# Performance work log

Measured on AMD Instinct MI355X. Metric: run time of the kernel, lower is better.

## Reference

```python
import jax, jax.numpy as jnp
import numpy as np

# config constants
B, S, H = 4, 2048, 1024
E = 8                 # n_routed_experts
M = 512               # moe_intermediate_size
K = 2                 # num_experts_per_tok
N_SHARED = 2
SM = M * N_SHARED     # shared expert intermediate
G = 64                # gene_size
GE_TEMP = 1.0
ALPHA = 0.001         # aux_loss_alpha
SEQ_AUX = True
NORM_TOPK = True
COS_TEMP = 0.78
CONS_ALPHA = 0.01
LEAKY_SLOPE = 0.01
EPS_COS = 1e-8


def setup_inputs() -> dict:
    key = jax.random.key(0)
    ks = jax.random.split(key, 12)
    sh = 1.0 / np.sqrt(H)
    sm = 1.0 / np.sqrt(M)
    ssm = 1.0 / np.sqrt(SM)
    sg = 1.0 / np.sqrt(G)
    return {
        "hidden_states": jax.random.normal(ks[0], (B, S, H), jnp.float32),
        "g": jax.random.normal(ks[1], (B, G), jnp.float32),
        "wt": jax.random.uniform(ks[2], (E, H), jnp.float32, -sh, sh),   # gate weight_token
        "wg": jax.random.uniform(ks[3], (E, G), jnp.float32, -sg, sg),   # gate weight_gene
        "w_gate": jax.random.uniform(ks[4], (E, H, M), jnp.float32, -sh, sh),
        "w_up": jax.random.uniform(ks[5], (E, H, M), jnp.float32, -sh, sh),
        "w_down": jax.random.uniform(ks[6], (E, M, H), jnp.float32, -sm, sm),
        "sw_gate": jax.random.uniform(ks[7], (H, SM), jnp.float32, -sh, sh),
        "sw_up": jax.random.uniform(ks[8], (H, SM), jnp.float32, -sh, sh),
        "sw_down": jax.random.uniform(ks[9], (SM, H), jnp.float32, -ssm, ssm),
    }


def _leaky(x):
    return jnp.where(x >= 0, x, LEAKY_SLOPE * x)


def _moe_forward(hidden_states, g, wt, wg, w_gate, w_up, w_down, sw_gate, sw_up, sw_down):
    b, s, h = hidden_states.shape
    x = hidden_states.reshape(-1, h)                    # [T, H], T = b*s
    T = x.shape[0]

    # ---- gate ----
    logits_h = x @ wt.T                                 # [T, E]
    logits_g = g @ wg.T                                 # [b, E]
    logits_g = jnp.repeat(logits_g, s, axis=0)          # [T, E]
    logits = (logits_h + logits_g / GE_TEMP) / (1.0 + 1.0 / GE_TEMP)
    scores = jax.nn.softmax(logits, axis=-1)            # [T, E]
    topk_w, topk_idx = jax.lax.top_k(scores, K)         # [T, K]
    if K > 1 and NORM_TOPK:
        topk_w = topk_w / (topk_w.sum(-1, keepdims=True) + 1e-20)

    # aux loss (seq_aux=True)
    onehot = jax.nn.one_hot(topk_idx.reshape(b, s * K), E, dtype=jnp.float32)  # [b, s*K, E]
    ce = onehot.sum(1) / (s * K / E)                    # [b, E]
    aux_loss = (ce * scores.reshape(b, s, E).mean(1)).sum(1).mean() * ALPHA

    # ---- routed experts: dense stacked compute, then gather ----
    gp = _leaky(jnp.einsum('th,ehm->etm', x, w_gate))   # [E, T, M]
    up = jnp.einsum('th,ehm->etm', x, w_up)
    y_all = jnp.einsum('etm,emh->eth', gp * up, w_down) # [E, T, H]
    y_sel = y_all[topk_idx, jnp.arange(T)[:, None], :]  # [T, K, H]
    y = (y_sel * topk_w[..., None]).sum(1).reshape(b, s, h)

    # ---- shared expert ----
    p = (_leaky(hidden_states @ sw_gate) * (hidden_states @ sw_up)) @ sw_down
    y = y + p

    # consistency cosine loss
    num = jnp.sum(y * p, -1)
    den = jnp.maximum(jnp.linalg.norm(y, axis=-1), EPS_COS) * jnp.maximum(jnp.linalg.norm(p, axis=-1), EPS_COS)
    closs = CONS_ALPHA * jnp.mean((num / den) / (1.0 + COS_TEMP))
    return y, aux_loss + closs


def reference(hidden_states, g, wt, wg, w_gate, w_up, w_down, sw_gate, sw_up, sw_down):
    y, _ = _moe_forward(hidden_states, g, wt, wg, w_gate, w_up, w_down, sw_gate, sw_up, sw_down)
    return y
```

## Files before the change

kernel.cpp:

```cpp
#include <hip/hip_runtime.h>
#include <stdint.h>

#define T_TOK 8192
#define H_DIM 1024
#define M_DIM 512
#define SM_DIM 1024
#define E_NUM 8
#define S_SEQ 2048
#define G_DIM 64
#define NASSIGN 16384
#define NSLOT (NASSIGN + E_NUM * 128)
#define MAX_TILES (NASSIGN / 128 + E_NUM)
#define NBLK_PLACE (NASSIGN / 256)

typedef float f32x4 __attribute__((ext_vector_type(4)));
typedef short bf16x8 __attribute__((ext_vector_type(8)));

struct TileDesc { int base; int expert; int nrows; };

#define WAITCNT_VM4 asm volatile("s_waitcnt vmcnt(4)" ::: "memory")
#define WAITCNT_VM0 asm volatile("s_waitcnt vmcnt(0)" ::: "memory")
#define WAITCNT_LGKM0 asm volatile("s_waitcnt lgkmcnt(0)" ::: "memory")

static __device__ __forceinline__ ushort f2b(float f) {
  union { float f; uint32_t u; } a; a.f = f;
  uint32_t r = a.u + 0x7fffu + ((a.u >> 16) & 1u);
  return (ushort)(r >> 16);
}
static __device__ __forceinline__ float b2f(ushort u) {
  union { uint32_t u; float f; } a; a.u = ((uint32_t)u) << 16;
  return a.f;
}
static __device__ __forceinline__ int imin(int a, int b) { return a < b ? a : b; }

static __device__ __forceinline__ void gll16(const void* g, void* l) {
  __builtin_amdgcn_global_load_lds(
      (const __attribute__((address_space(1))) void*)g,
      (__attribute__((address_space(3))) void*)l, 16, 0, 0);
}
static __device__ __forceinline__ int swz(int row) { return (row >> 1) & 3; }
static __device__ __forceinline__ int xcd_remap(int wg, int nwg) {
  return (wg & 7) * (nwg >> 3) + (wg >> 3);
}

__global__ void cvt_x_kernel(const float* __restrict__ x, ushort* __restrict__ xb) {
  int i = blockIdx.x * 256 + threadIdx.x;
  const float4 v = ((const float4*)x)[i];
  ushort4 o;
  o.x = f2b(v.x); o.y = f2b(v.y); o.z = f2b(v.z); o.w = f2b(v.w);
  ((ushort4*)xb)[i] = o;
}

__global__ void tcvt_kernel(const float* __restrict__ src, ushort* __restrict__ dst, int R, int C) {
  __shared__ float tile[32][33];
  size_t bo = (size_t)blockIdx.z * R * C;
  src += bo; dst += bo;
  int c0 = blockIdx.x * 32, r0 = blockIdx.y * 32;
#pragma unroll
  for (int i = 0; i < 4; ++i)
    tile[threadIdx.y + i * 8][threadIdx.x] =
        src[(size_t)(r0 + threadIdx.y + i * 8) * C + c0 + threadIdx.x];
  __syncthreads();
#pragma unroll
  for (int i = 0; i < 4; ++i)
    dst[(size_t)(c0 + threadIdx.y + i * 8) * R + r0 + threadIdx.x] =
        f2b(tile[threadIdx.x][threadIdx.y + i * 8]);
}

__global__ void lg_kernel(const float* __restrict__ g, const float* __restrict__ wg,
                          float* __restrict__ lg) {
  int tid = threadIdx.x;
  if (tid < 4 * E_NUM) {
    int b = tid >> 3, e = tid & 7;
    float s = 0.f;
    for (int i = 0; i < G_DIM; ++i) s += g[b * G_DIM + i] * wg[e * G_DIM + i];
    lg[tid] = s;
  }
}

__global__ __launch_bounds__(64) void router_kernel(
    const float* __restrict__ x, const float* __restrict__ wt, const float* __restrict__ lg,
    int* __restrict__ tidx, float* __restrict__ tw) {
  int t = blockIdx.x;
  int lane = threadIdx.x;
  const float* xr = x + (size_t)t * H_DIM;
  float a[E_NUM];
#pragma unroll
  for (int e = 0; e < E_NUM; ++e) a[e] = 0.f;
  for (int i = lane; i < H_DIM; i += 64) {
    float xv = xr[i];
#pragma unroll
    for (int e = 0; e < E_NUM; ++e) a[e] += xv * wt[e * H_DIM + i];
  }
#pragma unroll
  for (int e = 0; e < E_NUM; ++e)
    for (int off = 32; off; off >>= 1) a[e] += __shfl_xor(a[e], off, 64);
  if (lane == 0) {
    int b = t / S_SEQ;
    float l[E_NUM];
#pragma unroll
    for (int e = 0; e < E_NUM; ++e) l[e] = 0.5f * (a[e] + lg[b * E_NUM + e]);
    int i1 = 0; float b1 = l[0];
#pragma unroll
    for (int e = 1; e < E_NUM; ++e) if (l[e] > b1) { b1 = l[e]; i1 = e; }
    int i2 = -1; float b2 = -1e30f;
#pragma unroll
    for (int e = 0; e < E_NUM; ++e) if (e != i1 && l[e] > b2) { b2 = l[e]; i2 = e; }
    float e2 = expf(b2 - b1);
    float inv = 1.f / (1.f + e2);
    tidx[t * 2] = i1; tidx[t * 2 + 1] = i2;
    tw[t * 2] = inv;  tw[t * 2 + 1] = e2 * inv;
  }
}

__global__ __launch_bounds__(256) void hist_kernel(const int* __restrict__ tidx,
                                                   int* __restrict__ bcount) {
  __shared__ int h[E_NUM];
  int tid = threadIdx.x;
  if (tid < E_NUM) h[tid] = 0;
  __syncthreads();
  atomicAdd(&h[tidx[blockIdx.x * 256 + tid]], 1);
  __syncthreads();
  if (tid < E_NUM) bcount[blockIdx.x * E_NUM + tid] = h[tid];
}

__global__ __launch_bounds__(64) void scan2_kernel(
    const int* __restrict__ bcount, int* __restrict__ boffs, int* __restrict__ offs,
    TileDesc* __restrict__ desc, int* __restrict__ ndesc) {
  __shared__ int cnt[E_NUM];
  __shared__ int off_s[E_NUM];
  int lane = threadIdx.x;
  if (lane < E_NUM) {
    int s = 0;
    for (int b = 0; b < NBLK_PLACE; ++b) s += bcount[b * E_NUM + lane];
    cnt[lane] = s;
  }
  __syncthreads();
  if (lane == 0) {
    int o = 0, nd = 0;
    for (int e = 0; e < E_NUM; ++e) {
      off_s[e] = o;
      offs[e] = o;
      int n = cnt[e];
      for (int tb = 0; tb < n; tb += 128) {
        desc[nd].base = o + tb; desc[nd].expert = e;
        desc[nd].nrows = imin(n - tb, 128);
        ++nd;
      }
      o += n;
    }
    offs[E_NUM] = o;
    *ndesc = nd;
  }
  __syncthreads();
  if (lane < E_NUM) {
    int run = off_s[lane];
    for (int b = 0; b < NBLK_PLACE; ++b) {
      boffs[b * E_NUM + lane] = run;
      run += bcount[b * E_NUM + lane];
    }
  }
}

__global__ __launch_bounds__(256) void place2_kernel(
    const int* __restrict__ tidx, const int* __restrict__ boffs,
    int* __restrict__ perm, int* __restrict__ slot_of) {
  __shared__ int wcnt[4][E_NUM];
  int tid = threadIdx.x, wv = tid >> 6, lane = tid & 63;
  int i = blockIdx.x * 256 + tid;
  int e = tidx[i];
  unsigned long long lower = (lane == 63) ? 0x7fffffffffffffffull : ((1ull << lane) - 1ull);
  int rank = 0;
#pragma unroll
  for (int ee = 0; ee < E_NUM; ++ee) {
    unsigned long long m = __ballot(e == ee);
    if (e == ee) rank = __popcll(m & lower);
    if (lane == 0) wcnt[wv][ee] = __popcll(m);
  }
  __syncthreads();
  int off = boffs[blockIdx.x * E_NUM + e];
  for (int w = 0; w < wv; ++w) off += wcnt[w][e];
  int pos = off + rank;
  perm[pos] = i >> 1;
  slot_of[i] = pos;
}

__global__ __launch_bounds__(256) void gemm_dual_kernel(
    const ushort* __restrict__ A, const ushort* __restrict__ B0t, const ushort* __restrict__ B1t,
    ushort* __restrict__ Hout, int Kd, int Nd, int ncols,
    const int* __restrict__ perm, const TileDesc* __restrict__ desc, const int* __restrict__ ndesc) {
  __shared__ ushort As[2][128 * 32];
  __shared__ ushort B0s[2][64 * 32];
  __shared__ ushort B1s[2][64 * 32];

  int id = xcd_remap(blockIdx.x, gridDim.x);
  int mt = id / ncols, n0 = (id % ncols) * 64;

  int rowbase, nrows;
  const ushort *b0g, *b1g;
  if (desc) {
    if (mt >= *ndesc) return;
    TileDesc d = desc[mt];
    rowbase = d.base; nrows = d.nrows;
    size_t wo = (size_t)d.expert * Nd * Kd;
    b0g = B0t + wo; b1g = B1t + wo;
  } else {
    rowbase = mt * 128; nrows = 128; b0g = B0t; b1g = B1t;
  }
  int tid = threadIdx.x;
  int wv = tid >> 6, lane = tid & 63;

  int l4 = lane >> 2, c = lane & 3;
  int a0 = wv * 16 + l4, a1 = a0 + 64;
  int ga0 = desc ? perm[rowbase + imin(a0, nrows - 1)] : (rowbase + a0);
  int ga1 = desc ? perm[rowbase + imin(a1, nrows - 1)] : (rowbase + a1);
  const ushort* ap0 = A + (size_t)ga0 * Kd + ((c ^ swz(a0)) << 3);
  const ushort* ap1 = A + (size_t)ga1 * Kd + ((c ^ swz(a1)) << 3);
  int br = wv * 16 + l4;
  const ushort* bp0 = b0g + (size_t)(n0 + br) * Kd + ((c ^ swz(br)) << 3);
  const ushort* bp1 = b1g + (size_t)(n0 + br) * Kd + ((c ^ swz(br)) << 3);

  int wr = wv >> 1, wc = wv & 1;
  int lr = lane & 15, cg = lane >> 4;

  f32x4 acc0[4][2], acc1[4][2];
#pragma unroll
  for (int m = 0; m < 4; ++m)
#pragma unroll
    for (int n = 0; n < 2; ++n) { acc0[m][n] = (f32x4){0.f,0.f,0.f,0.f}; acc1[m][n] = (f32x4){0.f,0.f,0.f,0.f}; }

  int nk = Kd >> 5;
  gll16(ap0, &As[0][wv * 512]); gll16(ap1, &As[0][(wv + 4) * 512]);
  gll16(bp0, &B0s[0][wv * 512]); gll16(bp1, &B1s[0][wv * 512]);
  ap0 += 32; ap1 += 32; bp0 += 32; bp1 += 32;

  for (int kt = 0; kt < nk; ++kt) {
    int cur = kt & 1, nxt = cur ^ 1;
    if (kt + 1 < nk) {
      gll16(ap0, &As[nxt][wv * 512]); gll16(ap1, &As[nxt][(wv + 4) * 512]);
      gll16(bp0, &B0s[nxt][wv * 512]); gll16(bp1, &B1s[nxt][wv * 512]);
      ap0 += 32; ap1 += 32; bp0 += 32; bp1 += 32;
      WAITCNT_VM4;
    } else {
      WAITCNT_VM0;
    }
    __builtin_amdgcn_s_barrier();
    bf16x8 af[4], bq0[2], bq1[2];
#pragma unroll
    for (int m = 0; m < 4; ++m) {
      int row = wr * 64 + m * 16 + lr;
      af[m] = *(const bf16x8*)&As[cur][row * 32 + ((cg ^ swz(row)) << 3)];
    }
#pragma unroll
    for (int n = 0; n < 2; ++n) {
      int row = wc * 32 + n * 16 + lr;
      bq0[n] = *(const bf16x8*)&B0s[cur][row * 32 + ((cg ^ swz(row)) << 3)];
      bq1[n] = *(const bf16x8*)&B1s[cur][row * 32 + ((cg ^ swz(row)) << 3)];
    }
    WAITCNT_LGKM0;
    __builtin_amdgcn_s_barrier();
#pragma unroll
    for (int m = 0; m < 4; ++m)
#pragma unroll
      for (int n = 0; n < 2; ++n) {
        acc0[m][n] = __builtin_amdgcn_mfma_f32_16x16x32_bf16(af[m], bq0[n], acc0[m][n], 0, 0, 0);
        acc1[m][n] = __builtin_amdgcn_mfma_f32_16x16x32_bf16(af[m], bq1[n], acc1[m][n], 0, 0, 0);
      }
  }
  int rq = cg * 4, cq = lr;
#pragma unroll
  for (int m = 0; m < 4; ++m)
#pragma unroll
    for (int n = 0; n < 2; ++n)
#pragma unroll
      for (int r = 0; r < 4; ++r) {
        int row = wr * 64 + m * 16 + rq + r;
        if (row < nrows) {
          float gv = acc0[m][n][r], uv = acc1[m][n][r];
          float hv = (gv >= 0.f ? gv : 0.01f * gv) * uv;
          int col = n0 + wc * 32 + n * 16 + cq;
          Hout[(size_t)(rowbase + row) * Nd + col] = f2b(hv);
        }
      }
}

template <int BF16OUT>
__global__ __launch_bounds__(256) void gemm_single_kernel(
    const ushort* __restrict__ A, const ushort* __restrict__ Bt, void* __restrict__ Out,
    int Kd, int Nd, int ncols, const TileDesc* __restrict__ desc, const int* __restrict__ ndesc) {
  __shared__ ushort As[2][128 * 32];
  __shared__ ushort Bs[2][128 * 32];

  int id = xcd_remap(blockIdx.x, gridDim.x);
  int mt = id / ncols, n0 = (id % ncols) * 128;

  int rowbase, nrows;
  const ushort* bg;
  if (desc) {
    if (mt >= *ndesc) return;
    TileDesc d = desc[mt];
    rowbase = d.base; nrows = d.nrows;
    bg = Bt + (size_t)d.expert * Nd * Kd;
  } else {
    rowbase = mt * 128; nrows = 128; bg = Bt;
  }
  int tid = threadIdx.x;
  int wv = tid >> 6, lane = tid & 63;

  int l4 = lane >> 2, c = lane & 3;
  int a0 = wv * 16 + l4, a1 = a0 + 64;
  const ushort* ap0 = A + (size_t)(rowbase + a0) * Kd + ((c ^ swz(a0)) << 3);
  const ushort* ap1 = A + (size_t)(rowbase + a1) * Kd + ((c ^ swz(a1)) << 3);
  const ushort* bp0 = bg + (size_t)(n0 + a0) * Kd + ((c ^ swz(a0)) << 3);
  const ushort* bp1 = bg + (size_t)(n0 + a1) * Kd + ((c ^ swz(a1)) << 3);

  int wr = wv >> 1, wc = wv & 1;
  int lr = lane & 15, cg = lane >> 4;

  f32x4 acc[4][4];
#pragma unroll
  for (int m = 0; m < 4; ++m)
#pragma unroll
    for (int n = 0; n < 4; ++n) acc[m][n] = (f32x4){0.f,0.f,0.f,0.f};

  int nk = Kd >> 5;
  gll16(ap0, &As[0][wv * 512]); gll16(ap1, &As[0][(wv + 4) * 512]);
  gll16(bp0, &Bs[0][wv * 512]); gll16(bp1, &Bs[0][(wv + 4) * 512]);
  ap0 += 32; ap1 += 32; bp0 += 32; bp1 += 32;

  for (int kt = 0; kt < nk; ++kt) {
    int cur = kt & 1, nxt = cur ^ 1;
    if (kt + 1 < nk) {
      gll16(ap0, &As[nxt][wv * 512]); gll16(ap1, &As[nxt][(wv + 4) * 512]);
      gll16(bp0, &Bs[nxt][wv * 512]); gll16(bp1, &Bs[nxt][(wv + 4) * 512]);
      ap0 += 32; ap1 += 32; bp0 += 32; bp1 += 32;
      WAITCNT_VM4;
    } else {
      WAITCNT_VM0;
    }
    __builtin_amdgcn_s_barrier();
    bf16x8 af[4], bfr[4];
#pragma unroll
    for (int m = 0; m < 4; ++m) {
      int row = wr * 64 + m * 16 + lr;
      af[m] = *(const bf16x8*)&As[cur][row * 32 + ((cg ^ swz(row)) << 3)];
    }
#pragma unroll
    for (int n = 0; n < 4; ++n) {
      int row = wc * 64 + n * 16 + lr;
      bfr[n] = *(const bf16x8*)&Bs[cur][row * 32 + ((cg ^ swz(row)) << 3)];
    }
    WAITCNT_LGKM0;
    __builtin_amdgcn_s_barrier();
#pragma unroll
    for (int m = 0; m < 4; ++m)
#pragma unroll
      for (int n = 0; n < 4; ++n)
        acc[m][n] = __builtin_amdgcn_mfma_f32_16x16x32_bf16(af[m], bfr[n], acc[m][n], 0, 0, 0);
  }
  int rq = cg * 4, cq = lr;
#pragma unroll
  for (int m = 0; m < 4; ++m)
#pragma unroll
    for (int n = 0; n < 4; ++n)
#pragma unroll
      for (int r = 0; r < 4; ++r) {
        int row = wr * 64 + m * 16 + rq + r;
        if (row < nrows) {
          int col = n0 + wc * 64 + n * 16 + cq;
          size_t o = (size_t)(rowbase + row) * Nd + col;
          if (BF16OUT) ((ushort*)Out)[o] = f2b(acc[m][n][r]);
          else ((float*)Out)[o] = acc[m][n][r];
        }
      }
}

__global__ void final_kernel(float* __restrict__ y, const ushort* __restrict__ ye,
                             const int* __restrict__ slot_of, const float* __restrict__ tw) {
  int i = blockIdx.x * 256 + threadIdx.x;
  int t = i >> 8;
  int c4 = (i & 255) * 4;
  int s0 = slot_of[t * 2], s1 = slot_of[t * 2 + 1];
  float w0 = tw[t * 2], w1 = tw[t * 2 + 1];
  float4 v = ((float4*)y)[i];
  ushort4 a = *(const ushort4*)(ye + (size_t)s0 * H_DIM + c4);
  ushort4 b = *(const ushort4*)(ye + (size_t)s1 * H_DIM + c4);
  v.x += w0 * b2f(a.x) + w1 * b2f(b.x);
  v.y += w0 * b2f(a.y) + w1 * b2f(b.y);
  v.z += w0 * b2f(a.z) + w1 * b2f(b.z);
  v.w += w0 * b2f(a.w) + w1 * b2f(b.w);
  ((float4*)y)[i] = v;
}

extern "C" void kernel_launch(void* const* d_in, const int* in_sizes, int n_in,
                              void* d_out, int out_size, void* d_ws, size_t ws_size,
                              hipStream_t stream) {
  const float* x       = (const float*)d_in[0];
  const float* g       = (const float*)d_in[1];
  const float* wt      = (const float*)d_in[2];
  const float* wg      = (const float*)d_in[3];
  const float* w_gate  = (const float*)d_in[4];
  const float* w_up    = (const float*)d_in[5];
  const float* w_down  = (const float*)d_in[6];
  const float* sw_gate = (const float*)d_in[7];
  const float* sw_up   = (const float*)d_in[8];
  const float* sw_down = (const float*)d_in[9];
  float* y = (float*)d_out;

  char* p = (char*)d_ws;
  auto alloc = [&](size_t bytes) -> char* {
    char* r = p;
    p += (bytes + 255) & ~(size_t)255;
    return r;
  };
  ushort* xb    = (ushort*)alloc((size_t)T_TOK * H_DIM * 2);
  ushort* wg_t  = (ushort*)alloc((size_t)E_NUM * M_DIM * H_DIM * 2);
  ushort* wu_t  = (ushort*)alloc((size_t)E_NUM * M_DIM * H_DIM * 2);
  ushort* wd_t  = (ushort*)alloc((size_t)E_NUM * H_DIM * M_DIM * 2);
  ushort* swg_t = (ushort*)alloc((size_t)SM_DIM * H_DIM * 2);
  ushort* swu_t = (ushort*)alloc((size_t)SM_DIM * H_DIM * 2);
  ushort* swd_t = (ushort*)alloc((size_t)H_DIM * SM_DIM * 2);
  float* lg     = (float*)alloc(4 * E_NUM * 4);
  int* tidx     = (int*)alloc(NASSIGN * 4);
  float* tw     = (float*)alloc(NASSIGN * 4);
  int* bcount   = (int*)alloc(NBLK_PLACE * E_NUM * 4);
  int* boffs    = (int*)alloc(NBLK_PLACE * E_NUM * 4);
  int* offs     = (int*)alloc((E_NUM + 1) * 4);
  int* ndesc    = (int*)alloc(4);
  int* perm     = (int*)alloc(NASSIGN * 4);
  int* slot_of  = (int*)alloc(NASSIGN * 4);
  TileDesc* desc = (TileDesc*)alloc(MAX_TILES * sizeof(TileDesc));
  ushort* h_e   = (ushort*)alloc((size_t)NSLOT * M_DIM * 2);
  ushort* hsh   = (ushort*)alloc((size_t)T_TOK * SM_DIM * 2);
  ushort* ye    = (ushort*)alloc((size_t)NSLOT * H_DIM * 2);
  (void)ws_size; (void)in_sizes; (void)n_in; (void)out_size;

  cvt_x_kernel<<<T_TOK * H_DIM / 4 / 256, 256, 0, stream>>>(x, xb);
  dim3 tb(32, 8);
  tcvt_kernel<<<dim3(M_DIM / 32, H_DIM / 32, E_NUM), tb, 0, stream>>>(w_gate, wg_t, H_DIM, M_DIM);
  tcvt_kernel<<<dim3(M_DIM / 32, H_DIM / 32, E_NUM), tb, 0, stream>>>(w_up, wu_t, H_DIM, M_DIM);
  tcvt_kernel<<<dim3(H_DIM / 32, M_DIM / 32, E_NUM), tb, 0, stream>>>(w_down, wd_t, M_DIM, H_DIM);
  tcvt_kernel<<<dim3(SM_DIM / 32, H_DIM / 32, 1), tb, 0, stream>>>(sw_gate, swg_t, H_DIM, SM_DIM);
  tcvt_kernel<<<dim3(SM_DIM / 32, H_DIM / 32, 1), tb, 0, stream>>>(sw_up, swu_t, H_DIM, SM_DIM);
  tcvt_kernel<<<dim3(H_DIM / 32, SM_DIM / 32, 1), tb, 0, stream>>>(sw_down, swd_t, SM_DIM, H_DIM);

  lg_kernel<<<1, 32, 0, stream>>>(g, wg, lg);
  router_kernel<<<T_TOK, 64, 0, stream>>>(x, wt, lg, tidx, tw);
  hist_kernel<<<NBLK_PLACE, 256, 0, stream>>>(tidx, bcount);
  scan2_kernel<<<1, 64, 0, stream>>>(bcount, boffs, offs, desc, ndesc);
  place2_kernel<<<NBLK_PLACE, 256, 0, stream>>>(tidx, boffs, perm, slot_of);

  gemm_dual_kernel<<<(T_TOK / 128) * (SM_DIM / 64), 256, 0, stream>>>(
      xb, swg_t, swu_t, hsh, H_DIM, SM_DIM, SM_DIM / 64, nullptr, nullptr, nullptr);
  gemm_single_kernel<0><<<(T_TOK / 128) * (H_DIM / 128), 256, 0, stream>>>(
      hsh, swd_t, (void*)y, SM_DIM, H_DIM, H_DIM / 128, nullptr, nullptr);

  gemm_dual_kernel<<<MAX_TILES * (M_DIM / 64), 256, 0, stream>>>(
      xb, wg_t, wu_t, h_e, H_DIM, M_DIM, M_DIM / 64, perm, desc, ndesc);
  gemm_single_kernel<1><<<MAX_TILES * (H_DIM / 128), 256, 0, stream>>>(
      h_e, wd_t, (void*)ye, M_DIM, H_DIM, H_DIM / 128, desc, ndesc);

  final_kernel<<<T_TOK * H_DIM / 4 / 256, 256, 0, stream>>>(y, ye, slot_of, tw);
}
```

Before: 241.5 us.

## Merge shared and routed GEMMs into combined launches with 256-row tiles and triple buffering

```diff
diff --git a/kernel.cpp b/kernel.cpp
--- a/kernel.cpp
+++ b/kernel.cpp
@@ -9,8 +9,8 @@
 #define S_SEQ 2048
 #define G_DIM 64
 #define NASSIGN 16384
-#define NSLOT (NASSIGN + E_NUM * 128)
-#define MAX_TILES (NASSIGN / 128 + E_NUM)
+#define NSLOT (NASSIGN + E_NUM * 256)
+#define MAX_TILES (NASSIGN / 256 + E_NUM)
 #define NBLK_PLACE (NASSIGN / 256)
 
 typedef float f32x4 __attribute__((ext_vector_type(4)));
@@ -19,6 +19,7 @@
 struct TileDesc { int base; int expert; int nrows; };
 
 #define WAITCNT_VM4 asm volatile("s_waitcnt vmcnt(4)" ::: "memory")
+#define WAITCNT_VM3 asm volatile("s_waitcnt vmcnt(3)" ::: "memory")
 #define WAITCNT_VM0 asm volatile("s_waitcnt vmcnt(0)" ::: "memory")
 #define WAITCNT_LGKM0 asm volatile("s_waitcnt lgkmcnt(0)" ::: "memory")
 
@@ -142,9 +143,9 @@
       off_s[e] = o;
       offs[e] = o;
       int n = cnt[e];
-      for (int tb = 0; tb < n; tb += 128) {
+      for (int tb = 0; tb < n; tb += 256) {
         desc[nd].base = o + tb; desc[nd].expert = e;
-        desc[nd].nrows = imin(n - tb, 128);
+        desc[nd].nrows = imin(n - tb, 256);
         ++nd;
       }
       o += n;
@@ -185,194 +186,218 @@
   slot_of[i] = pos;
 }
 
-__global__ __launch_bounds__(256) void gemm_dual_kernel(
-    const ushort* __restrict__ A, const ushort* __restrict__ B0t, const ushort* __restrict__ B1t,
-    ushort* __restrict__ Hout, int Kd, int Nd, int ncols,
-    const int* __restrict__ perm, const TileDesc* __restrict__ desc, const int* __restrict__ ndesc) {
-  __shared__ ushort As[2][128 * 32];
-  __shared__ ushort B0s[2][64 * 32];
-  __shared__ ushort B1s[2][64 * 32];
-
+template <int DUAL>
+static __device__ __forceinline__ void gemm_core(
+    const ushort* __restrict__ A, const ushort* __restrict__ B0,
+    const ushort* __restrict__ B1, void* __restrict__ Out, int outf32,
+    int Kd, int NdOut, int rowbase, int nrows, int n0,
+    const int* __restrict__ perm, ushort* Asb, ushort* Bsb) {
+  constexpr int BN = DUAL ? 256 : 128;
+  constexpr int BSTRIDE = BN * 32;
+  int tid = threadIdx.x, wv = tid >> 6, lane = tid & 63;
+  int sr = tid >> 2, sc = tid & 3;
+  int r1 = sr + 128;
+
+  int ga0 = perm ? perm[rowbase + imin(sr, nrows - 1)] : (rowbase + sr);
+  int ga1 = perm ? perm[rowbase + imin(r1, nrows - 1)] : (rowbase + r1);
+  const ushort* ap0 = A + (size_t)ga0 * Kd + ((sc ^ swz(sr)) << 3);
+  const ushort* ap1 = A + (size_t)ga1 * Kd + ((sc ^ swz(r1)) << 3);
+  const ushort* bp0;
+  const ushort* bp1 = nullptr;
+  if (DUAL) {
+    int rb0 = n0 + sr, rb1 = n0 + r1;
+    const ushort* s0 = ((rb0 >> 4) & 1) ? B1 : B0;
+    const ushort* s1 = ((rb1 >> 4) & 1) ? B1 : B0;
+    bp0 = s0 + (size_t)(((rb0 >> 5) << 4) + (rb0 & 15)) * Kd + ((sc ^ swz(sr)) << 3);
+    bp1 = s1 + (size_t)(((rb1 >> 5) << 4) + (rb1 & 15)) * Kd + ((sc ^ swz(r1)) << 3);
+  } else {
+    bp0 = B0 + (size_t)(n0 + sr) * Kd + ((sc ^ swz(sr)) << 3);
+  }
+
+  auto stageA = [&](int b) {
+    ushort* ad = Asb + b * 8192 + wv * 512;
+    gll16(ap0, ad); gll16(ap1, ad + 4096);
+    ap0 += 32; ap1 += 32;
+  };
+  auto stageB = [&](int b) {
+    ushort* bd = Bsb + b * BSTRIDE + wv * 512;
+    gll16(bp0, bd); bp0 += 32;
+    if (DUAL) { gll16(bp1, bd + 4096); bp1 += 32; }
+  };
+
+  int wr = wv >> 2, wc = wv & 3;
+  int lr = lane & 15, cg = lane >> 4;
+
+  constexpr int NF = DUAL ? 4 : 2;
+  f32x4 acc[8][NF];
+#pragma unroll
+  for (int m = 0; m < 8; ++m)
+#pragma unroll
+    for (int n = 0; n < NF; ++n) acc[m][n] = (f32x4){0.f, 0.f, 0.f, 0.f};
+
+  int nk = Kd >> 5;
+  stageA(0); stageB(0);
+  stageA(1); stageB(1);
+  if (DUAL) WAITCNT_VM4; else WAITCNT_VM3;
+  __builtin_amdgcn_s_barrier();
+
+  for (int kt = 0; kt < nk; ++kt) {
+    int b = kt % 3;
+    const ushort* abuf = Asb + b * 8192;
+    const ushort* bbuf = Bsb + b * BSTRIDE;
+    bool pf = (kt + 2 < nk);
+    int b2 = (kt + 2) % 3;
+
+    if (DUAL) {
+      bf16x8 af[8];
+#pragma unroll
+      for (int m = 0; m < 8; ++m) {
+        int row = wr * 128 + m * 16 + lr;
+        af[m] = *(const bf16x8*)(abuf + row * 32 + ((cg ^ swz(row)) << 3));
+      }
+      bf16x8 bq[2];
+#pragma unroll
+      for (int n = 0; n < 2; ++n) {
+        int row = wc * 64 + n * 16 + lr;
+        bq[n] = *(const bf16x8*)(bbuf + row * 32 + ((cg ^ swz(row)) << 3));
+      }
+      if (pf) stageA(b2);
+      __builtin_amdgcn_s_setprio(1);
+#pragma unroll
+      for (int m = 0; m < 8; ++m) {
+        acc[m][0] = __builtin_amdgcn_mfma_f32_16x16x32_bf16(af[m], bq[0], acc[m][0], 0, 0, 0);
+        acc[m][1] = __builtin_amdgcn_mfma_f32_16x16x32_bf16(af[m], bq[1], acc[m][1], 0, 0, 0);
+      }
+      __builtin_amdgcn_s_setprio(0);
+      bf16x8 bq2[2];
+#pragma unroll
+      for (int n = 0; n < 2; ++n) {
+        int row = wc * 64 + (n + 2) * 16 + lr;
+        bq2[n] = *(const bf16x8*)(bbuf + row * 32 + ((cg ^ swz(row)) << 3));
+      }
+      if (pf) stageB(b2);
+      __builtin_amdgcn_s_setprio(1);
+#pragma unroll
+      for (int m = 0; m < 8; ++m) {
+        acc[m][2] = __builtin_amdgcn_mfma_f32_16x16x32_bf16(af[m], bq2[0], acc[m][2], 0, 0, 0);
+        acc[m][3] = __builtin_amdgcn_mfma_f32_16x16x32_bf16(af[m], bq2[1], acc[m][3], 0, 0, 0);
+      }
+      __builtin_amdgcn_s_setprio(0);
+    } else {
+      bf16x8 bq[2];
+#pragma unroll
+      for (int n = 0; n < 2; ++n) {
+        int row = wc * 32 + n * 16 + lr;
+        bq[n] = *(const bf16x8*)(bbuf + row * 32 + ((cg ^ swz(row)) << 3));
+      }
+      bf16x8 af[4];
+#pragma unroll
+      for (int m = 0; m < 4; ++m) {
+        int row = wr * 128 + m * 16 + lr;
+        af[m] = *(const bf16x8*)(abuf + row * 32 + ((cg ^ swz(row)) << 3));
+      }
+      if (pf) { stageA(b2); stageB(b2); }
+      __builtin_amdgcn_s_setprio(1);
+#pragma unroll
+      for (int m = 0; m < 4; ++m) {
+        acc[m][0] = __builtin_amdgcn_mfma_f32_16x16x32_bf16(af[m], bq[0], acc[m][0], 0, 0, 0);
+        acc[m][1] = __builtin_amdgcn_mfma_f32_16x16x32_bf16(af[m], bq[1], acc[m][1], 0, 0, 0);
+      }
+      __builtin_amdgcn_s_setprio(0);
+      bf16x8 af2[4];
+#pragma unroll
+      for (int m = 0; m < 4; ++m) {
+        int row = wr * 128 + (m + 4) * 16 + lr;
+        af2[m] = *(const bf16x8*)(abuf + row * 32 + ((cg ^ swz(row)) << 3));
+      }
+      __builtin_amdgcn_s_setprio(1);
+#pragma unroll
+      for (int m = 0; m < 4; ++m) {
+        acc[m + 4][0] = __builtin_amdgcn_mfma_f32_16x16x32_bf16(af2[m], bq[0], acc[m + 4][0], 0, 0, 0);
+        acc[m + 4][1] = __builtin_amdgcn_mfma_f32_16x16x32_bf16(af2[m], bq[1], acc[m + 4][1], 0, 0, 0);
+      }
+      __builtin_amdgcn_s_setprio(0);
+    }
+    WAITCNT_LGKM0;
+    if (pf) { if (DUAL) WAITCNT_VM4; else WAITCNT_VM3; }
+    else WAITCNT_VM0;
+    __builtin_amdgcn_s_barrier();
+  }
+
+  int rq = cg * 4, cq = lr;
+  if (DUAL) {
+#pragma unroll
+    for (int m = 0; m < 8; ++m)
+#pragma unroll
+      for (int p = 0; p < 2; ++p)
+#pragma unroll
+        for (int r = 0; r < 4; ++r) {
+          int row = wr * 128 + m * 16 + rq + r;
+          if (row < nrows) {
+            float gv = acc[m][2 * p][r], uv = acc[m][2 * p + 1][r];
+            float hv = (gv >= 0.f ? gv : 0.01f * gv) * uv;
+            int col = (n0 >> 1) + wc * 32 + p * 16 + cq;
+            ((ushort*)Out)[(size_t)(rowbase + row) * NdOut + col] = f2b(hv);
+          }
+        }
+  } else {
+#pragma unroll
+    for (int m = 0; m < 8; ++m)
+#pragma unroll
+      for (int n = 0; n < 2; ++n)
+#pragma unroll
+        for (int r = 0; r < 4; ++r) {
+          int row = wr * 128 + m * 16 + rq + r;
+          if (row < nrows) {
+            int col = n0 + wc * 32 + n * 16 + cq;
+            size_t o = (size_t)(rowbase + row) * NdOut + col;
+            if (outf32) ((float*)Out)[o] = acc[m][n][r];
+            else ((ushort*)Out)[o] = f2b(acc[m][n][r]);
+          }
+        }
+  }
+}
+
+__global__ __launch_bounds__(512) void gemm_dual_all(
+    const ushort* __restrict__ xb, const ushort* __restrict__ swg,
+    const ushort* __restrict__ swu, ushort* __restrict__ hsh,
+    const ushort* __restrict__ wg, const ushort* __restrict__ wu,
+    ushort* __restrict__ h_e, const int* __restrict__ perm,
+    const TileDesc* __restrict__ desc, const int* __restrict__ ndesc) {
+  __shared__ ushort Asb[3 * 8192];
+  __shared__ ushort Bsb[3 * 8192];
   int id = xcd_remap(blockIdx.x, gridDim.x);
-  int mt = id / ncols, n0 = (id % ncols) * 64;
-
-  int rowbase, nrows;
-  const ushort *b0g, *b1g;
-  if (desc) {
+  if (id < 256) {
+    int mt = id >> 3, n0 = (id & 7) * 256;
+    gemm_core<1>(xb, swg, swu, hsh, 0, H_DIM, SM_DIM, mt * 256, 256, n0, nullptr, Asb, Bsb);
+  } else {
+    int rid = id - 256;
+    int mt = rid >> 2, n0 = (rid & 3) * 256;
     if (mt >= *ndesc) return;
     TileDesc d = desc[mt];
-    rowbase = d.base; nrows = d.nrows;
-    size_t wo = (size_t)d.expert * Nd * Kd;
-    b0g = B0t + wo; b1g = B1t + wo;
+    size_t wo = (size_t)d.expert * M_DIM * H_DIM;
+    gemm_core<1>(xb, wg + wo, wu + wo, h_e, 0, H_DIM, M_DIM, d.base, d.nrows, n0, perm, Asb, Bsb);
+  }
+}
+
+__global__ __launch_bounds__(512) void gemm_down_all(
+    const ushort* __restrict__ hsh, const ushort* __restrict__ swd, float* __restrict__ y,
+    const ushort* __restrict__ h_e, const ushort* __restrict__ wd, ushort* __restrict__ ye,
+    const TileDesc* __restrict__ desc, const int* __restrict__ ndesc) {
+  __shared__ ushort Asb[3 * 8192];
+  __shared__ ushort Bsb[3 * 4096];
+  int id = xcd_remap(blockIdx.x, gridDim.x);
+  if (id < 256) {
+    int mt = id >> 3, n0 = (id & 7) * 128;
+    gemm_core<0>(hsh, swd, nullptr, (void*)y, 1, SM_DIM, H_DIM, mt * 256, 256, n0, nullptr, Asb, Bsb);
   } else {
-    rowbase = mt * 128; nrows = 128; b0g = B0t; b1g = B1t;
-  }
-  int tid = threadIdx.x;
-  int wv = tid >> 6, lane = tid & 63;
-
-  int l4 = lane >> 2, c = lane & 3;
-  int a0 = wv * 16 + l4, a1 = a0 + 64;
-  int ga0 = desc ? perm[rowbase + imin(a0, nrows - 1)] : (rowbase + a0);
-  int ga1 = desc ? perm[rowbase + imin(a1, nrows - 1)] : (rowbase + a1);
-  const ushort* ap0 = A + (size_t)ga0 * Kd + ((c ^ swz(a0)) << 3);
-  const ushort* ap1 = A + (size_t)ga1 * Kd + ((c ^ swz(a1)) << 3);
-  int br = wv * 16 + l4;
-  const ushort* bp0 = b0g + (size_t)(n0 + br) * Kd + ((c ^ swz(br)) << 3);
-  const ushort* bp1 = b1g + (size_t)(n0 + br) * Kd + ((c ^ swz(br)) << 3);
-
-  int wr = wv >> 1, wc = wv & 1;
-  int lr = lane & 15, cg = lane >> 4;
-
-  f32x4 acc0[4][2], acc1[4][2];
-#pragma unroll
-  for (int m = 0; m < 4; ++m)
-#pragma unroll
-    for (int n = 0; n < 2; ++n) { acc0[m][n] = (f32x4){0.f,0.f,0.f,0.f}; acc1[m][n] = (f32x4){0.f,0.f,0.f,0.f}; }
-
-  int nk = Kd >> 5;
-  gll16(ap0, &As[0][wv * 512]); gll16(ap1, &As[0][(wv + 4) * 512]);
-  gll16(bp0, &B0s[0][wv * 512]); gll16(bp1, &B1s[0][wv * 512]);
-  ap0 += 32; ap1 += 32; bp0 += 32; bp1 += 32;
-
-  for (int kt = 0; kt < nk; ++kt) {
-    int cur = kt & 1, nxt = cur ^ 1;
-    if (kt + 1 < nk) {
-      gll16(ap0, &As[nxt][wv * 512]); gll16(ap1, &As[nxt][(wv + 4) * 512]);
-      gll16(bp0, &B0s[nxt][wv * 512]); gll16(bp1, &B1s[nxt][wv * 512]);
-      ap0 += 32; ap1 += 32; bp0 += 32; bp1 += 32;
-      WAITCNT_VM4;
-    } else {
-      WAITCNT_VM0;
-    }
-    __builtin_amdgcn_s_barrier();
-    bf16x8 af[4], bq0[2], bq1[2];
-#pragma unroll
-    for (int m = 0; m < 4; ++m) {
-      int row = wr * 64 + m * 16 + lr;
-      af[m] = *(const bf16x8*)&As[cur][row * 32 + ((cg ^ swz(row)) << 3)];
-    }
-#pragma unroll
-    for (int n = 0; n < 2; ++n) {
-      int row = wc * 32 + n * 16 + lr;
-      bq0[n] = *(const bf16x8*)&B0s[cur][row * 32 + ((cg ^ swz(row)) << 3)];
-      bq1[n] = *(const bf16x8*)&B1s[cur][row * 32 + ((cg ^ swz(row)) << 3)];
-    }
-    WAITCNT_LGKM0;
-    __builtin_amdgcn_s_barrier();
-#pragma unroll
-    for (int m = 0; m < 4; ++m)
-#pragma unroll
-      for (int n = 0; n < 2; ++n) {
-        acc0[m][n] = __builtin_amdgcn_mfma_f32_16x16x32_bf16(af[m], bq0[n], acc0[m][n], 0, 0, 0);
-        acc1[m][n] = __builtin_amdgcn_mfma_f32_16x16x32_bf16(af[m], bq1[n], acc1[m][n], 0, 0, 0);
-      }
-  }
-  int rq = cg * 4, cq = lr;
-#pragma unroll
-  for (int m = 0; m < 4; ++m)
-#pragma unroll
-    for (int n = 0; n < 2; ++n)
-#pragma unroll
-      for (int r = 0; r < 4; ++r) {
-        int row = wr * 64 + m * 16 + rq + r;
-        if (row < nrows) {
-          float gv = acc0[m][n][r], uv = acc1[m][n][r];
-          float hv = (gv >= 0.f ? gv : 0.01f * gv) * uv;
-          int col = n0 + wc * 32 + n * 16 + cq;
-          Hout[(size_t)(rowbase + row) * Nd + col] = f2b(hv);
-        }
-      }
-}
-
-template <int BF16OUT>
-__global__ __launch_bounds__(256) void gemm_single_kernel(
-    const ushort* __restrict__ A, const ushort* __restrict__ Bt, void* __restrict__ Out,
-    int Kd, int Nd, int ncols, const TileDesc* __restrict__ desc, const int* __restrict__ ndesc) {
-  __shared__ ushort As[2][128 * 32];
-  __shared__ ushort Bs[2][128 * 32];
-
-  int id = xcd_remap(blockIdx.x, gridDim.x);
-  int mt = id / ncols, n0 = (id % ncols) * 128;
-
-  int rowbase, nrows;
-  const ushort* bg;
-  if (desc) {
+    int rid = id - 256;
+    int mt = rid >> 3, n0 = (rid & 7) * 128;
     if (mt >= *ndesc) return;
     TileDesc d = desc[mt];
-    rowbase = d.base; nrows = d.nrows;
-    bg = Bt + (size_t)d.expert * Nd * Kd;
-  } else {
-    rowbase = mt * 128; nrows = 128; bg = Bt;
-  }
-  int tid = threadIdx.x;
-  int wv = tid >> 6, lane = tid & 63;
-
-  int l4 = lane >> 2, c = lane & 3;
-  int a0 = wv * 16 + l4, a1 = a0 + 64;
-  const ushort* ap0 = A + (size_t)(rowbase + a0) * Kd + ((c ^ swz(a0)) << 3);
-  const ushort* ap1 = A + (size_t)(rowbase + a1) * Kd + ((c ^ swz(a1)) << 3);
-  const ushort* bp0 = bg + (size_t)(n0 + a0) * Kd + ((c ^ swz(a0)) << 3);
-  const ushort* bp1 = bg + (size_t)(n0 + a1) * Kd + ((c ^ swz(a1)) << 3);
-
-  int wr = wv >> 1, wc = wv & 1;
-  int lr = lane & 15, cg = lane >> 4;
-
-  f32x4 acc[4][4];
-#pragma unroll
-  for (int m = 0; m < 4; ++m)
-#pragma unroll
-    for (int n = 0; n < 4; ++n) acc[m][n] = (f32x4){0.f,0.f,0.f,0.f};
-
-  int nk = Kd >> 5;
-  gll16(ap0, &As[0][wv * 512]); gll16(ap1, &As[0][(wv + 4) * 512]);
-  gll16(bp0, &Bs[0][wv * 512]); gll16(bp1, &Bs[0][(wv + 4) * 512]);
-  ap0 += 32; ap1 += 32; bp0 += 32; bp1 += 32;
-
-  for (int kt = 0; kt < nk; ++kt) {
-    int cur = kt & 1, nxt = cur ^ 1;
-    if (kt + 1 < nk) {
-      gll16(ap0, &As[nxt][wv * 512]); gll16(ap1, &As[nxt][(wv + 4) * 512]);
-      gll16(bp0, &Bs[nxt][wv * 512]); gll16(bp1, &Bs[nxt][(wv + 4) * 512]);
-      ap0 += 32; ap1 += 32; bp0 += 32; bp1 += 32;
-      WAITCNT_VM4;
-    } else {
-      WAITCNT_VM0;
-    }
-    __builtin_amdgcn_s_barrier();
-    bf16x8 af[4], bfr[4];
-#pragma unroll
-    for (int m = 0; m < 4; ++m) {
-      int row = wr * 64 + m * 16 + lr;
-      af[m] = *(const bf16x8*)&As[cur][row * 32 + ((cg ^ swz(row)) << 3)];
-    }
-#pragma unroll
-    for (int n = 0; n < 4; ++n) {
-      int row = wc * 64 + n * 16 + lr;
-      bfr[n] = *(const bf16x8*)&Bs[cur][row * 32 + ((cg ^ swz(row)) << 3)];
-    }
-    WAITCNT_LGKM0;
-    __builtin_amdgcn_s_barrier();
-#pragma unroll
-    for (int m = 0; m < 4; ++m)
-#pragma unroll
-      for (int n = 0; n < 4; ++n)
-        acc[m][n] = __builtin_amdgcn_mfma_f32_16x16x32_bf16(af[m], bfr[n], acc[m][n], 0, 0, 0);
-  }
-  int rq = cg * 4, cq = lr;
-#pragma unroll
-  for (int m = 0; m < 4; ++m)
-#pragma unroll
-    for (int n = 0; n < 4; ++n)
-#pragma unroll
-      for (int r = 0; r < 4; ++r) {
-        int row = wr * 64 + m * 16 + rq + r;
-        if (row < nrows) {
-          int col = n0 + wc * 64 + n * 16 + cq;
-          size_t o = (size_t)(rowbase + row) * Nd + col;
-          if (BF16OUT) ((ushort*)Out)[o] = f2b(acc[m][n][r]);
-          else ((float*)Out)[o] = acc[m][n][r];
-        }
-      }
+    gemm_core<0>(h_e, wd + (size_t)d.expert * H_DIM * M_DIM, nullptr, (void*)ye, 0,
+                 M_DIM, H_DIM, d.base, d.nrows, n0, nullptr, Asb, Bsb);
+  }
 }
 
 __global__ void final_kernel(float* __restrict__ y, const ushort* __restrict__ ye,
@@ -450,15 +475,10 @@
   scan2_kernel<<<1, 64, 0, stream>>>(bcount, boffs, offs, desc, ndesc);
   place2_kernel<<<NBLK_PLACE, 256, 0, stream>>>(tidx, boffs, perm, slot_of);
 
-  gemm_dual_kernel<<<(T_TOK / 128) * (SM_DIM / 64), 256, 0, stream>>>(
-      xb, swg_t, swu_t, hsh, H_DIM, SM_DIM, SM_DIM / 64, nullptr, nullptr, nullptr);
-  gemm_single_kernel<0><<<(T_TOK / 128) * (H_DIM / 128), 256, 0, stream>>>(
-      hsh, swd_t, (void*)y, SM_DIM, H_DIM, H_DIM / 128, nullptr, nullptr);
-
-  gemm_dual_kernel<<<MAX_TILES * (M_DIM / 64), 256, 0, stream>>>(
-      xb, wg_t, wu_t, h_e, H_DIM, M_DIM, M_DIM / 64, perm, desc, ndesc);
-  gemm_single_kernel<1><<<MAX_TILES * (H_DIM / 128), 256, 0, stream>>>(
-      h_e, wd_t, (void*)ye, M_DIM, H_DIM, H_DIM / 128, desc, ndesc);
+  gemm_dual_all<<<256 + MAX_TILES * 4, 512, 0, stream>>>(
+      xb, swg_t, swu_t, hsh, wg_t, wu_t, h_e, perm, desc, ndesc);
+  gemm_down_all<<<256 + MAX_TILES * 8, 512, 0, stream>>>(
+      hsh, swd_t, y, h_e, wd_t, ye, desc, ndesc);
 
   final_kernel<<<T_TOK * H_DIM / 4 / 256, 256, 0, stream>>>(y, ye, slot_of, tw);
 }
```

Measured after the change: 233.3 us. 1.04x faster.
